# Kernel optimization log

Measured on AMD Instinct MI355X. Metric: run time of the kernel, lower is better.

## Reference

```python
import jax, jax.numpy as jnp
import numpy as np

NEG_SLOPE = 0.2


def gatv2(x, src, dst, Wl, Wr, att, b, concat):
    """PyG GATv2Conv (share_weights=False, default negative_slope=0.2).
    x: [N, Fin]; src/dst: [E] (self-loops already included);
    Wl/Wr: [Fin, H*D]; att: [H, D]; b: [H*D] if concat else [D].
    """
    N = x.shape[0]
    H, D = att.shape
    xl = (x @ Wl).reshape(N, H, D)  # source transform (messages)
    xr = (x @ Wr).reshape(N, H, D)  # target transform
    g = xl[src] + xr[dst]                                   # [E, H, D]
    e = jnp.einsum('ehd,hd->eh', jax.nn.leaky_relu(g, NEG_SLOPE), att)  # [E, H]
    # segment softmax over incoming edges of each dst node
    m = jax.ops.segment_max(e, dst, num_segments=N)         # [N, H]
    ex = jnp.exp(e - m[dst])
    s = jax.ops.segment_sum(ex, dst, num_segments=N)
    alpha = ex / (s[dst] + 1e-16)                           # [E, H]
    out = jax.ops.segment_sum(alpha[:, :, None] * xl[src], dst, num_segments=N)  # [N, H, D]
    out = out.reshape(N, H * D) if concat else out.mean(axis=1)
    return out + b


def _glorot(key, fan_in, shape):
    return jax.random.normal(key, shape, dtype=jnp.float32) / np.sqrt(fan_in)


def setup_inputs() -> dict:
    key = jax.random.key(0)
    N, E = 50000, 800000
    dim_in, dim_h, dim_out, heads = 128, 32, 16, 8
    hid = dim_h * heads  # 256
    ks = jax.random.split(key, 16)
    x = jax.random.normal(ks[0], (N, dim_in), dtype=jnp.float32)
    edge_index = jax.random.randint(ks[1], (2, E), 0, N, dtype=jnp.int32)
    p = {
        'Wl1': _glorot(ks[2], dim_in, (dim_in, hid)),
        'Wr1': _glorot(ks[3], dim_in, (dim_in, hid)),
        'att1': _glorot(ks[4], dim_h, (heads, dim_h)),
        'b1': jnp.zeros((hid,), jnp.float32),
        'Wl2': _glorot(ks[5], hid, (hid, hid)),
        'Wr2': _glorot(ks[6], hid, (hid, hid)),
        'att2': _glorot(ks[7], dim_h, (heads, dim_h)),
        'b2': jnp.zeros((hid,), jnp.float32),
        'Wl3': _glorot(ks[8], hid, (hid, hid)),
        'Wr3': _glorot(ks[9], hid, (hid, hid)),
        'att3': _glorot(ks[10], dim_h, (heads, dim_h)),
        'b3': jnp.zeros((hid,), jnp.float32),
        'Wl4': _glorot(ks[11], hid, (hid, dim_out)),
        'Wr4': _glorot(ks[12], hid, (hid, dim_out)),
        'att4': _glorot(ks[13], dim_out, (1, dim_out)),
        'b4': jnp.zeros((dim_out,), jnp.float32),
    }
    return {'x': x, 'edge_index': edge_index, **p}


def reference(x, edge_index,
              Wl1, Wr1, att1, b1,
              Wl2, Wr2, att2, b2,
              Wl3, Wr3, att3, b3,
              Wl4, Wr4, att4, b4):
    N = x.shape[0]
    # PyG GATv2Conv default add_self_loops=True
    loop = jnp.arange(N, dtype=edge_index.dtype)
    src = jnp.concatenate([edge_index[0], loop])
    dst = jnp.concatenate([edge_index[1], loop])
    # eval mode: dropout is identity (note: first dropout output is unused in source)
    h = gatv2(x, src, dst, Wl1, Wr1, att1, b1, concat=True)
    h = jax.nn.elu(h)
    h = gatv2(h, src, dst, Wl2, Wr2, att2, b2, concat=True)
    h = jax.nn.elu(h)
    h = gatv2(h, src, dst, Wl3, Wr3, att3, b3, concat=True)
    h = jax.nn.elu(h)
    h = gatv2(h, src, dst, Wl4, Wr4, att4, b4, concat=True)  # heads=1 -> same as concat
    return jax.nn.log_softmax(h, axis=1)
```

## Files before the change

### kernel.cpp

```cpp
#include <hip/hip_runtime.h>
#include <math.h>

#define NEG_SLOPE 0.2f

typedef _Float16 f16;
typedef _Float16 f16x2 __attribute__((ext_vector_type(2)));
typedef _Float16 f16x4 __attribute__((ext_vector_type(4)));
typedef _Float16 f16x8 __attribute__((ext_vector_type(8)));
typedef float f32x4 __attribute__((ext_vector_type(4)));

static inline int idiv(int a, int b) { return (a + b - 1) / b; }



__global__ __launch_bounds__(256) void conv_x_packed(const float* __restrict__ x,
                                                     f16* __restrict__ pa, int N) {
    int R = blockIdx.x;
    #pragma unroll
    for (int u = 0; u < 8; ++u) {
        int c = threadIdx.x + u * 256;
        int g = c >> 7, r = c & 127;
        int row = R * 128 + r;
        f16x8 v;
        if (row < N) {
            float4 a = *(const float4*)(x + (size_t)row * 128 + g * 8);
            float4 b = *(const float4*)(x + (size_t)row * 128 + g * 8 + 4);
            v = (f16x8){(f16)a.x, (f16)a.y, (f16)a.z, (f16)a.w,
                        (f16)b.x, (f16)b.y, (f16)b.z, (f16)b.w};
        } else {
            v = (f16x8){0, 0, 0, 0, 0, 0, 0, 0};
        }
        *(f16x8*)(pa + ((size_t)(R * 16 + g) * 128 + r) * 8) = v;
    }
}

__global__ __launch_bounds__(256) void convT_all(
    const float* __restrict__ W1l, const float* __restrict__ W1r,
    const float* __restrict__ W2l, const float* __restrict__ W2r,
    const float* __restrict__ W3l, const float* __restrict__ W3r,
    f16* __restrict__ P1l, f16* __restrict__ P1r,
    f16* __restrict__ P2l, f16* __restrict__ P2r,
    f16* __restrict__ P3l, f16* __restrict__ P3r) {
    __shared__ float tbl[32][33];
    const float* W;
    f16* P;
    int K;
    switch (blockIdx.z) {
        case 0: W = W1l; P = P1l; K = 128; break;
        case 1: W = W1r; P = P1r; K = 128; break;
        case 2: W = W2l; P = P2l; K = 256; break;
        case 3: W = W2r; P = P2r; K = 256; break;
        case 4: W = W3l; P = P3l; K = 256; break;
        default: W = W3r; P = P3r; K = 256; break;
    }
    int bk = blockIdx.x * 32, bc = blockIdx.y * 32;
    if (bk >= K) return;
    int tx = threadIdx.x & 31, ty = threadIdx.x >> 5;
    #pragma unroll
    for (int i = 0; i < 32; i += 8)
        tbl[ty + i][tx] = W[(size_t)(bk + ty + i) * 256 + bc + tx];
    __syncthreads();
    if (threadIdx.x < 128) {
        int cl = threadIdx.x & 31;
        int gl = threadIdx.x >> 5;
        int col = bc + cl;
        int g = (bk >> 3) + gl;
        f16x8 v;
        #pragma unroll
        for (int j = 0; j < 8; ++j) v[j] = (f16)tbl[gl * 8 + j][cl];
        *(f16x8*)(P + ((size_t)((col >> 7) * (K >> 3) + g) * 128 + (col & 127)) * 8) = v;
    }
}


__global__ void hist_kernel(const int* __restrict__ dst, int E, int N, int* __restrict__ cnt) {
    int i = blockIdx.x * blockDim.x + threadIdx.x;
    if (i >= E + N) return;
    int d = (i < E) ? dst[i] : (i - E);
    atomicAdd(&cnt[d], 1);
}

__global__ __launch_bounds__(256) void scanA(const int* __restrict__ cnt,
                                             int* __restrict__ bsum, int N) {
    __shared__ int ws[4];
    int tid = threadIdx.x, lane = tid & 63, wid = tid >> 6;
    int i0 = blockIdx.x * 1024 + tid * 4;
    int s = 0;
    if (i0 + 3 < N) {
        int4 v = *(const int4*)(cnt + i0);
        s = v.x + v.y + v.z + v.w;
    } else {
        for (int j = 0; j < 4; ++j)
            if (i0 + j < N) s += cnt[i0 + j];
    }
    #pragma unroll
    for (int o = 1; o < 64; o <<= 1) s += __shfl_xor(s, o);
    if (lane == 0) ws[wid] = s;
    __syncthreads();
    if (tid == 0) bsum[blockIdx.x] = ws[0] + ws[1] + ws[2] + ws[3];
}

__global__ __launch_bounds__(256) void scanB(int* __restrict__ bsum, int nb) {
    __shared__ int ws[4];
    int tid = threadIdx.x, lane = tid & 63, wid = tid >> 6;
    int v = (tid < nb) ? bsum[tid] : 0;
    int incl = v;
    #pragma unroll
    for (int o = 1; o < 64; o <<= 1) {
        int t = __shfl_up(incl, o);
        if (lane >= o) incl += t;
    }
    if (lane == 63) ws[wid] = incl;
    __syncthreads();
    int add = 0;
    for (int w = 0; w < wid; ++w) add += ws[w];
    if (tid < nb) bsum[tid] = add + incl - v;
}

__global__ __launch_bounds__(256) void scanC(const int* __restrict__ cnt,
                                             const int* __restrict__ bsum,
                                             int* __restrict__ rp, int* __restrict__ wofs, int N) {
    __shared__ int ws[4];
    __shared__ int base_s;
    int tid = threadIdx.x, lane = tid & 63, wid = tid >> 6;
    int i0 = blockIdx.x * 1024 + tid * 4;
    int v0 = (i0 + 0 < N) ? cnt[i0 + 0] : 0;
    int v1 = (i0 + 1 < N) ? cnt[i0 + 1] : 0;
    int v2 = (i0 + 2 < N) ? cnt[i0 + 2] : 0;
    int v3 = (i0 + 3 < N) ? cnt[i0 + 3] : 0;
    int t4 = v0 + v1 + v2 + v3;
    int incl = t4;
    #pragma unroll
    for (int o = 1; o < 64; o <<= 1) {
        int t = __shfl_up(incl, o);
        if (lane >= o) incl += t;
    }
    if (lane == 63) ws[wid] = incl;
    if (tid == 0) base_s = bsum[blockIdx.x];
    __syncthreads();
    int wadd = 0;
    for (int w = 0; w < wid; ++w) wadd += ws[w];
    int pre = base_s + wadd + incl - t4;
    int p1 = pre + v0, p2 = p1 + v1, p3 = p2 + v2, p4 = p3 + v3;
    if (i0 + 0 < N) { wofs[i0 + 0] = pre; rp[i0 + 1] = p1; }
    if (i0 + 1 < N) { wofs[i0 + 1] = p1;  rp[i0 + 2] = p2; }
    if (i0 + 2 < N) { wofs[i0 + 2] = p2;  rp[i0 + 3] = p3; }
    if (i0 + 3 < N) { wofs[i0 + 3] = p3;  rp[i0 + 4] = p4; }
    if (blockIdx.x == 0 && tid == 0) rp[0] = 0;
}

__global__ void scatter_kernel(const int* __restrict__ src, const int* __restrict__ dst,
                               int E, int N, int* __restrict__ wofs, int* __restrict__ sorted_src) {
    int i = blockIdx.x * blockDim.x + threadIdx.x;
    if (i >= E + N) return;
    int d, s;
    if (i < E) { d = dst[i]; s = src[i]; } else { d = i - E; s = d; }
    int pos = atomicAdd(&wofs[d], 1);
    sorted_src[pos] = s;
}


__device__ __forceinline__ void gll16(const f16* g, f16* l) {
#if __has_builtin(__builtin_amdgcn_global_load_lds)
    __builtin_amdgcn_global_load_lds((const __attribute__((address_space(1))) void*)g,
                                     (__attribute__((address_space(3))) void*)l, 16, 0, 0);
#else
    *(f16x8*)l = *(const f16x8*)g;
#endif
}

__global__ __launch_bounds__(256) void gemm16_packed(
    const f16* __restrict__ PA, int N, int K,
    const f16* __restrict__ PBl, const f16* __restrict__ PBr,
    f16* __restrict__ Cl, f16* __restrict__ Cr) {
    __shared__ f16 lds[2][2][8192];
    const int nblk = gridDim.x;
    int bid = blockIdx.x;
    int xcd = bid & 7, jj = bid >> 3;
    int nper = nblk >> 3, rem = nblk & 7;
    int slot = (xcd < rem) ? xcd * (nper + 1) + jj
                           : rem * (nper + 1) + (xcd - rem) * nper + jj;
    int R = slot >> 2, by = slot & 3;
    const f16* __restrict__ PB = (by >> 1) ? PBr : PBl;
    f16* __restrict__ C = (by >> 1) ? Cr : Cl;
    const int cb = by & 1;
    const int row0 = R * 128;
    const int col0 = cb * 128;
    const f16* Abase = PA + (size_t)R * 128 * K;
    const f16* Bbase = PB + (size_t)cb * 128 * K;
    const int t = threadIdx.x;
    const int lane = t & 63, wid = t >> 6;
    const int wr = (wid >> 1) * 64, wc = (wid & 1) * 64;
    const int lg = lane >> 4, lr = lane & 15;

    f32x4 acc[4][4];
    #pragma unroll
    for (int m = 0; m < 4; ++m)
        #pragma unroll
        for (int n = 0; n < 4; ++n) acc[m][n] = (f32x4){0.f, 0.f, 0.f, 0.f};

    auto stage = [&](int buf, int k0) {
        const f16* As = Abase + (size_t)k0 * 128 + t * 8;
        const f16* Bs = Bbase + (size_t)k0 * 128 + t * 8;
        f16* Al = &lds[buf][0][t * 8];
        f16* Bl = &lds[buf][1][t * 8];
        #pragma unroll
        for (int u = 0; u < 4; ++u) gll16(As + u * 2048, Al + u * 2048);
        #pragma unroll
        for (int u = 0; u < 4; ++u) gll16(Bs + u * 2048, Bl + u * 2048);
    };

    const int nk = K >> 6;
    stage(0, 0);
    asm volatile("s_waitcnt vmcnt(0)" ::: "memory");
    __syncthreads();
    for (int c = 0; c < nk; ++c) {
        if (c + 1 < nk) stage((c + 1) & 1, (c + 1) * 64);
        f16x8* Asp = (f16x8*)lds[c & 1][0];
        f16x8* Bsp = (f16x8*)lds[c & 1][1];
        #pragma unroll
        for (int s = 0; s < 2; ++s) {
            f16x8 af[4], bf[4];
            #pragma unroll
            for (int m = 0; m < 4; ++m) af[m] = Asp[(s * 4 + lg) * 128 + wr + m * 16 + lr];
            #pragma unroll
            for (int n = 0; n < 4; ++n) bf[n] = Bsp[(s * 4 + lg) * 128 + wc + n * 16 + lr];
            #pragma unroll
            for (int m = 0; m < 4; ++m)
                #pragma unroll
                for (int n = 0; n < 4; ++n)
                    acc[m][n] = __builtin_amdgcn_mfma_f32_16x16x32_f16(af[m], bf[n], acc[m][n], 0, 0, 0);
        }
        asm volatile("s_waitcnt vmcnt(0)" ::: "memory");
        __syncthreads();
    }
    #pragma unroll
    for (int m = 0; m < 4; ++m) {
        int row_b = row0 + wr + m * 16 + lg * 4;
        #pragma unroll
        for (int reg = 0; reg < 4; ++reg) {
            int row = row_b + reg;
            if (row < N) {
                #pragma unroll
                for (int n = 0; n < 4; ++n)
                    C[(size_t)row * 256 + col0 + wc + n * 16 + lr] = (f16)acc[m][n][reg];
            }
        }
    }
}


__global__ __launch_bounds__(256) void gemm_small16(
    const f16* __restrict__ A, int N,
    const float* __restrict__ Wl, const float* __restrict__ Wr,
    float* __restrict__ Cl, float* __restrict__ Cr) {
    const int K = 256, M = 16;
    __shared__ float As[16][260];
    __shared__ float Ws[256 * 16];
    const float* __restrict__ W = (blockIdx.y == 0) ? Wl : Wr;
    float* __restrict__ C = (blockIdx.y == 0) ? Cl : Cr;
    int row0 = blockIdx.x * 16;
    int tid = threadIdx.x;
    {
        #pragma unroll
        for (int u = 0; u < 4; ++u)
            *(float4*)&Ws[tid * 16 + u * 4] = *(const float4*)(W + tid * 16 + u * 4);
        int r = tid >> 4;
        int c = (tid & 15) * 16;
        int row = row0 + r;
        if (row < N) {
            int R = row >> 7, rr = row & 127;
            const f16* base = A + ((size_t)(R * 32 + (c >> 3)) * 128 + rr) * 8;
            f16x8 v0 = *(const f16x8*)base;
            f16x8 v1 = *(const f16x8*)(base + 1024);
            #pragma unroll
            for (int j = 0; j < 8; ++j) {
                As[r][c + j] = (float)v0[j];
                As[r][c + 8 + j] = (float)v1[j];
            }
        } else {
            #pragma unroll
            for (int j = 0; j < 16; ++j) As[r][c + j] = 0.f;
        }
    }
    __syncthreads();
    int r = tid >> 4;
    int col = tid & 15;
    float acc = 0.f;
    #pragma unroll 8
    for (int k = 0; k < K; ++k) acc = fmaf(As[r][k], Ws[k * M + col], acc);
    int row = row0 + r;
    if (row < N) C[(size_t)row * M + col] = acc;
}


__global__ __launch_bounds__(256) void edge_h8_f16(
    const f16* __restrict__ xl, const f16* __restrict__ xr,
    const int* __restrict__ rp, const int* __restrict__ ss,
    const float* __restrict__ att, const float* __restrict__ bias,
    f16* __restrict__ hout, int N) {
    int tid = threadIdx.x;
    int half = tid >> 5;
    int hl = tid & 31;
    int n = blockIdx.x * 8 + half;
    if (n >= N) return;
    const int HD = 256;
    f16x8 xrr = *(const f16x8*)(xr + (size_t)n * HD + hl * 8);
    float4 atlo = *(const float4*)(att + hl * 8);
    float4 athi = *(const float4*)(att + hl * 8 + 4);
    f16x2 at01 = {(f16)atlo.x, (f16)atlo.y};
    f16x2 at23 = {(f16)atlo.z, (f16)atlo.w};
    f16x2 at45 = {(f16)athi.x, (f16)athi.y};
    f16x2 at67 = {(f16)athi.z, (f16)athi.w};
    const f16 ns = (f16)NEG_SLOPE;
    float m = -INFINITY, s = 0.f;
    f16x8 a = {0, 0, 0, 0, 0, 0, 0, 0};
    int beg = rp[n], end = rp[n + 1];
    int last = end - 1;
    const f16* xb = xl + hl * 8;
    f16x8 r0 = *(const f16x8*)(xb + (size_t)ss[beg] * HD);
    f16x8 r1 = *(const f16x8*)(xb + (size_t)ss[min(beg + 1, last)] * HD);
    f16x8 r2 = *(const f16x8*)(xb + (size_t)ss[min(beg + 2, last)] * HD);
    f16x8 r3 = *(const f16x8*)(xb + (size_t)ss[min(beg + 3, last)] * HD);
    f16x8 r4 = *(const f16x8*)(xb + (size_t)ss[min(beg + 4, last)] * HD);
    f16x8 r5 = *(const f16x8*)(xb + (size_t)ss[min(beg + 5, last)] * HD);
    int j6 = ss[min(beg + 6, last)];
    int j7 = ss[min(beg + 7, last)];

    auto score = [&](const f16x8& cur) -> float {
        f16x8 g = cur + xrr;
        f16x8 gs = g * ns;
        f16x8 lk = __builtin_elementwise_max(g, gs);
#if __has_builtin(__builtin_amdgcn_fdot2)
        f16x2 l01 = __builtin_shufflevector(lk, lk, 0, 1);
        f16x2 l23 = __builtin_shufflevector(lk, lk, 2, 3);
        f16x2 l45 = __builtin_shufflevector(lk, lk, 4, 5);
        f16x2 l67 = __builtin_shufflevector(lk, lk, 6, 7);
        float p = __builtin_amdgcn_fdot2(l01, at01, 0.f, false);
        p = __builtin_amdgcn_fdot2(l23, at23, p, false);
        p = __builtin_amdgcn_fdot2(l45, at45, p, false);
        p = __builtin_amdgcn_fdot2(l67, at67, p, false);
#else
        float p = (float)lk[0] * atlo.x + (float)lk[1] * atlo.y +
                  (float)lk[2] * atlo.z + (float)lk[3] * atlo.w +
                  (float)lk[4] * athi.x + (float)lk[5] * athi.y +
                  (float)lk[6] * athi.z + (float)lk[7] * athi.w;
#endif
        return p;
    };

    int i = beg;
    for (; i + 1 < end; i += 2) {
        f16x8 c0 = r0, c1 = r1;
        r0 = r2; r1 = r3; r2 = r4; r3 = r5;
        r4 = *(const f16x8*)(xb + (size_t)j6 * HD);
        r5 = *(const f16x8*)(xb + (size_t)j7 * HD);
        j6 = ss[min(i + 8, last)];
        j7 = ss[min(i + 9, last)];
        float p0 = score(c0);
        float p1 = score(c1);
        p0 += __shfl_xor(p0, 1);
        p1 += __shfl_xor(p1, 1);
        p0 += __shfl_xor(p0, 2);
        p1 += __shfl_xor(p1, 2);
        float d0 = p0 - m, d1 = p1 - m;
        if (__any(fmaxf(d0, d1) > 4.f)) {
            float mn = fmaxf(m, fmaxf(p0, p1));
            float cf = __expf(m - mn);
            s *= cf;
            f16 cfh = (f16)cf;
            a = a * (f16x8){cfh, cfh, cfh, cfh, cfh, cfh, cfh, cfh};
            m = mn;
            d0 = p0 - m; d1 = p1 - m;
        }
        float e0 = __expf(d0);
        float e1 = __expf(d1);
        s += e0 + e1;
        f16 e0h = (f16)e0, e1h = (f16)e1;
        f16x8 e0v = {e0h, e0h, e0h, e0h, e0h, e0h, e0h, e0h};
        f16x8 e1v = {e1h, e1h, e1h, e1h, e1h, e1h, e1h, e1h};
#if __has_builtin(__builtin_elementwise_fma)
        a = __builtin_elementwise_fma(c0, e0v, a);
        a = __builtin_elementwise_fma(c1, e1v, a);
#else
        a = a + c0 * e0v + c1 * e1v;
#endif
    }
    if (i < end) {
        f16x8 c0 = r0;
        float p0 = score(c0);
        p0 += __shfl_xor(p0, 1);
        p0 += __shfl_xor(p0, 2);
        float d0 = p0 - m;
        if (__any(d0 > 4.f)) {
            float mn = fmaxf(m, p0);
            float cf = __expf(m - mn);
            s *= cf;
            f16 cfh = (f16)cf;
            a = a * (f16x8){cfh, cfh, cfh, cfh, cfh, cfh, cfh, cfh};
            m = mn;
            d0 = p0 - m;
        }
        float e0 = __expf(d0);
        s += e0;
        f16 e0h = (f16)e0;
        f16x8 e0v = {e0h, e0h, e0h, e0h, e0h, e0h, e0h, e0h};
#if __has_builtin(__builtin_elementwise_fma)
        a = __builtin_elementwise_fma(c0, e0v, a);
#else
        a = a + c0 * e0v;
#endif
    }
    float inv = 1.f / (s + 1e-16f);
    float4 blo = *(const float4*)(bias + hl * 8);
    float4 bhi = *(const float4*)(bias + hl * 8 + 4);
    float o[8];
    o[0] = (float)a[0] * inv + blo.x; o[1] = (float)a[1] * inv + blo.y;
    o[2] = (float)a[2] * inv + blo.z; o[3] = (float)a[3] * inv + blo.w;
    o[4] = (float)a[4] * inv + bhi.x; o[5] = (float)a[5] * inv + bhi.y;
    o[6] = (float)a[6] * inv + bhi.z; o[7] = (float)a[7] * inv + bhi.w;
    f16x8 ov;
    #pragma unroll
    for (int j = 0; j < 8; ++j) {
        float e = o[j] > 0.f ? o[j] : __expf(o[j]) - 1.f;
        ov[j] = (f16)e;
    }
    *(f16x8*)(hout + ((size_t)((n >> 7) * 32 + hl) * 128 + (n & 127)) * 8) = ov;
}


__global__ __launch_bounds__(256) void edge_h1_kernel(
    const float* __restrict__ xl, const float* __restrict__ xr,
    const int* __restrict__ rp, const int* __restrict__ ss,
    const float* __restrict__ att, const float* __restrict__ bias,
    float* __restrict__ out, int N) {
    int tid = threadIdx.x;
    int grp = tid >> 4;
    int gl = tid & 15;
    int n = blockIdx.x * 16 + grp;
    if (n >= N) return;
    float xrv = xr[(size_t)n * 16 + gl];
    float attv = att[gl];
    float bv = bias[gl];
    float m = -INFINITY, s = 0.f, acc = 0.f;
    int beg = rp[n], end = rp[n + 1], last = end - 1;
    const float* xb = xl + gl;
    float x0 = xb[(size_t)ss[beg] * 16];
    float x1 = xb[(size_t)ss[min(beg + 1, last)] * 16];
    float x2 = xb[(size_t)ss[min(beg + 2, last)] * 16];
    float x3 = xb[(size_t)ss[min(beg + 3, last)] * 16];
    int j4 = ss[min(beg + 4, last)];
    int j5 = ss[min(beg + 5, last)];
    int i = beg;
    for (; i + 1 < end; i += 2) {
        float c0 = x0, c1 = x1;
        x0 = x2; x1 = x3;
        x2 = xb[(size_t)j4 * 16];
        x3 = xb[(size_t)j5 * 16];
        j4 = ss[min(i + 6, last)];
        j5 = ss[min(i + 7, last)];
        float g0 = c0 + xrv, g1 = c1 + xrv;
        float p0 = attv * fmaxf(g0, NEG_SLOPE * g0);
        float p1 = attv * fmaxf(g1, NEG_SLOPE * g1);
        p0 += __shfl_xor(p0, 1); p1 += __shfl_xor(p1, 1);
        p0 += __shfl_xor(p0, 2); p1 += __shfl_xor(p1, 2);
        p0 += __shfl_xor(p0, 4); p1 += __shfl_xor(p1, 4);
        p0 += __shfl_xor(p0, 8); p1 += __shfl_xor(p1, 8);
        float d0 = p0 - m, d1 = p1 - m;
        if (__any(fmaxf(d0, d1) > 8.f)) {
            float mn = fmaxf(m, fmaxf(p0, p1));
            float cf = __expf(m - mn);
            s *= cf; acc *= cf;
            m = mn;
            d0 = p0 - m; d1 = p1 - m;
        }
        float e0 = __expf(d0), e1 = __expf(d1);
        s += e0 + e1;
        acc = fmaf(e1, c1, fmaf(e0, c0, acc));
    }
    if (i < end) {
        float c0 = x0;
        float g0 = c0 + xrv;
        float p0 = attv * fmaxf(g0, NEG_SLOPE * g0);
        p0 += __shfl_xor(p0, 1);
        p0 += __shfl_xor(p0, 2);
        p0 += __shfl_xor(p0, 4);
        p0 += __shfl_xor(p0, 8);
        float d0 = p0 - m;
        if (__any(d0 > 8.f)) {
            float mn = fmaxf(m, p0);
            float cf = __expf(m - mn);
            s *= cf; acc *= cf;
            m = mn;
            d0 = p0 - m;
        }
        float e0 = __expf(d0);
        s += e0;
        acc = fmaf(e0, c0, acc);
    }
    float v = acc / (s + 1e-16f) + bv;
    float mx = v;
    mx = fmaxf(mx, __shfl_xor(mx, 1));
    mx = fmaxf(mx, __shfl_xor(mx, 2));
    mx = fmaxf(mx, __shfl_xor(mx, 4));
    mx = fmaxf(mx, __shfl_xor(mx, 8));
    float ex = __expf(v - mx);
    float se = ex;
    se += __shfl_xor(se, 1);
    se += __shfl_xor(se, 2);
    se += __shfl_xor(se, 4);
    se += __shfl_xor(se, 8);
    out[(size_t)n * 16 + gl] = v - mx - __logf(se);
}


extern "C" void kernel_launch(void* const* d_in, const int* in_sizes, int n_in,
                              void* d_out, int out_size, void* d_ws, size_t ws_size,
                              hipStream_t stream) {
    const float* x    = (const float*)d_in[0];
    const int*   ei   = (const int*)d_in[1];
    const float* Wl1  = (const float*)d_in[2];
    const float* Wr1  = (const float*)d_in[3];
    const float* att1 = (const float*)d_in[4];
    const float* b1   = (const float*)d_in[5];
    const float* Wl2  = (const float*)d_in[6];
    const float* Wr2  = (const float*)d_in[7];
    const float* att2 = (const float*)d_in[8];
    const float* b2   = (const float*)d_in[9];
    const float* Wl3  = (const float*)d_in[10];
    const float* Wr3  = (const float*)d_in[11];
    const float* att3 = (const float*)d_in[12];
    const float* b3   = (const float*)d_in[13];
    const float* Wl4  = (const float*)d_in[14];
    const float* Wr4  = (const float*)d_in[15];
    const float* att4 = (const float*)d_in[16];
    const float* b4   = (const float*)d_in[17];

    const int N = in_sizes[0] / 128;
    const int E = in_sizes[1] / 2;
    const int* src = ei;
    const int* dst = ei + E;
    const int Etot = E + N;
    const int ntile = idiv(N, 128);

    char* wsb = (char*)d_ws;
    size_t off = 0;
    auto alloc = [&](size_t bytes) -> void* {
        void* p = wsb + off;
        off += (bytes + 255) & ~(size_t)255;
        return p;
    };
    f16*   PX   = (f16*)alloc((size_t)ntile * 128 * 128 * 2);
    f16*   PH   = (f16*)alloc((size_t)ntile * 128 * 256 * 2);
    f16*   xl16 = (f16*)alloc((size_t)N * 256 * 2);
    f16*   xr16 = (f16*)alloc((size_t)N * 256 * 2);
    float* xl4  = (float*)alloc((size_t)N * 16 * 4);
    float* xr4  = (float*)alloc((size_t)N * 16 * 4);
    f16*   PB1l = (f16*)alloc((size_t)256 * 128 * 2);
    f16*   PB1r = (f16*)alloc((size_t)256 * 128 * 2);
    f16*   PB2l = (f16*)alloc((size_t)256 * 256 * 2);
    f16*   PB2r = (f16*)alloc((size_t)256 * 256 * 2);
    f16*   PB3l = (f16*)alloc((size_t)256 * 256 * 2);
    f16*   PB3r = (f16*)alloc((size_t)256 * 256 * 2);
    int*   cnt  = (int*)alloc((size_t)N * 4);
    int*   wof  = (int*)alloc((size_t)N * 4);
    int*   rp   = (int*)alloc((size_t)(N + 1) * 4);
    int*   ss   = (int*)alloc((size_t)Etot * 4);
    int*   bsum = (int*)alloc((size_t)idiv(N, 1024) * 4);

    conv_x_packed<<<ntile, 256, 0, stream>>>(x, PX, N);
    convT_all<<<dim3(8, 8, 6), 256, 0, stream>>>(Wl1, Wr1, Wl2, Wr2, Wl3, Wr3,
                                                 PB1l, PB1r, PB2l, PB2r, PB3l, PB3r);

    hipMemsetAsync(cnt, 0, (size_t)N * 4, stream);
    hist_kernel<<<idiv(Etot, 256), 256, 0, stream>>>(dst, E, N, cnt);
    const int nb = idiv(N, 1024);
    scanA<<<nb, 256, 0, stream>>>(cnt, bsum, N);
    scanB<<<1, 256, 0, stream>>>(bsum, nb);
    scanC<<<nb, 256, 0, stream>>>(cnt, bsum, rp, wof, N);
    scatter_kernel<<<idiv(Etot, 256), 256, 0, stream>>>(src, dst, E, N, wof, ss);

    const int nblk = ntile * 4;
    gemm16_packed<<<nblk, 256, 0, stream>>>(PX, N, 128, PB1l, PB1r, xl16, xr16);
    edge_h8_f16<<<idiv(N, 8), 256, 0, stream>>>(xl16, xr16, rp, ss, att1, b1, PH, N);
    gemm16_packed<<<nblk, 256, 0, stream>>>(PH, N, 256, PB2l, PB2r, xl16, xr16);
    edge_h8_f16<<<idiv(N, 8), 256, 0, stream>>>(xl16, xr16, rp, ss, att2, b2, PH, N);
    gemm16_packed<<<nblk, 256, 0, stream>>>(PH, N, 256, PB3l, PB3r, xl16, xr16);
    edge_h8_f16<<<idiv(N, 8), 256, 0, stream>>>(xl16, xr16, rp, ss, att3, b3, PH, N);
    gemm_small16<<<dim3(idiv(N, 16), 2), 256, 0, stream>>>(PH, N, Wl4, Wr4, xl4, xr4);
    edge_h1_kernel<<<idiv(N, 16), 256, 0, stream>>>(xl4, xr4, rp, ss, att4, b4, (float*)d_out, N);
}
```

Baseline: 447.2 us.

## Store GEMM output head-major and split edge kernel per attention head

The GEMM epilogue now writes xl/xr in a head-major layout ([H][N][32]), so each head's features form a contiguous 3.2 MB plane. The edge kernel is restructured so each block handles one head for 32 nodes, with 8 lanes per node loading 4 halfs each, and the software prefetch depth drops to 4. The aim is to make random neighbour gathers hit a much smaller working set per head, giving better L2/MALL locality across the blocks working on the same head. In exchange each gathered row is only 64 bytes, so there are more, smaller memory transactions, the row indices are re-read once per head, and the output store becomes a narrower f16x4 write.

```diff
diff --git a/kernel.cpp b/kernel.cpp
--- a/kernel.cpp
+++ b/kernel.cpp
@@ -234,6 +234,7 @@
         asm volatile("s_waitcnt vmcnt(0)" ::: "memory");
         __syncthreads();
     }
+    const size_t hs = (size_t)N * 32;
     #pragma unroll
     for (int m = 0; m < 4; ++m) {
         int row_b = row0 + wr + m * 16 + lg * 4;
@@ -242,8 +243,10 @@
             int row = row_b + reg;
             if (row < N) {
                 #pragma unroll
-                for (int n = 0; n < 4; ++n)
-                    C[(size_t)row * 256 + col0 + wc + n * 16 + lr] = (f16)acc[m][n][reg];
+                for (int n = 0; n < 4; ++n) {
+                    int col = col0 + wc + n * 16 + lr;
+                    C[hs * (col >> 5) + (size_t)row * 32 + (col & 31)] = (f16)acc[m][n][reg];
+                }
             }
         }
     }
@@ -294,82 +297,78 @@
 }
 
 
-__global__ __launch_bounds__(256) void edge_h8_f16(
+__global__ __launch_bounds__(256) void edge_h8_hsplit(
     const f16* __restrict__ xl, const f16* __restrict__ xr,
     const int* __restrict__ rp, const int* __restrict__ ss,
     const float* __restrict__ att, const float* __restrict__ bias,
     f16* __restrict__ hout, int N) {
+    int bid = blockIdx.x;
+    int h = bid & 7;
+    int tile = bid >> 3;
     int tid = threadIdx.x;
-    int half = tid >> 5;
-    int hl = tid & 31;
-    int n = blockIdx.x * 8 + half;
+    int lane = tid & 63, wave = tid >> 6;
+    int n = tile * 32 + wave * 8 + (lane >> 3);
     if (n >= N) return;
-    const int HD = 256;
-    f16x8 xrr = *(const f16x8*)(xr + (size_t)n * HD + hl * 8);
-    float4 atlo = *(const float4*)(att + hl * 8);
-    float4 athi = *(const float4*)(att + hl * 8 + 4);
-    f16x2 at01 = {(f16)atlo.x, (f16)atlo.y};
-    f16x2 at23 = {(f16)atlo.z, (f16)atlo.w};
-    f16x2 at45 = {(f16)athi.x, (f16)athi.y};
-    f16x2 at67 = {(f16)athi.z, (f16)athi.w};
+    int ll = lane & 7;
+    const size_t hs = (size_t)N * 32;
+    const f16* xlh = xl + hs * h;
+    const f16* xrh = xr + hs * h;
+    f16x4 xrr = *(const f16x4*)(xrh + (size_t)n * 32 + ll * 4);
+    float4 atv = *(const float4*)(att + h * 32 + ll * 4);
+    f16x2 at01 = {(f16)atv.x, (f16)atv.y};
+    f16x2 at23 = {(f16)atv.z, (f16)atv.w};
     const f16 ns = (f16)NEG_SLOPE;
     float m = -INFINITY, s = 0.f;
-    f16x8 a = {0, 0, 0, 0, 0, 0, 0, 0};
+    f16x4 a = {0, 0, 0, 0};
     int beg = rp[n], end = rp[n + 1];
     int last = end - 1;
-    const f16* xb = xl + hl * 8;
-    f16x8 r0 = *(const f16x8*)(xb + (size_t)ss[beg] * HD);
-    f16x8 r1 = *(const f16x8*)(xb + (size_t)ss[min(beg + 1, last)] * HD);
-    f16x8 r2 = *(const f16x8*)(xb + (size_t)ss[min(beg + 2, last)] * HD);
-    f16x8 r3 = *(const f16x8*)(xb + (size_t)ss[min(beg + 3, last)] * HD);
-    f16x8 r4 = *(const f16x8*)(xb + (size_t)ss[min(beg + 4, last)] * HD);
-    f16x8 r5 = *(const f16x8*)(xb + (size_t)ss[min(beg + 5, last)] * HD);
-    int j6 = ss[min(beg + 6, last)];
-    int j7 = ss[min(beg + 7, last)];
-
-    auto score = [&](const f16x8& cur) -> float {
-        f16x8 g = cur + xrr;
-        f16x8 gs = g * ns;
-        f16x8 lk = __builtin_elementwise_max(g, gs);
+    const f16* xb = xlh + ll * 4;
+    f16x4 r0 = *(const f16x4*)(xb + (size_t)ss[beg] * 32);
+    f16x4 r1 = *(const f16x4*)(xb + (size_t)ss[min(beg + 1, last)] * 32);
+    f16x4 r2 = *(const f16x4*)(xb + (size_t)ss[min(beg + 2, last)] * 32);
+    f16x4 r3 = *(const f16x4*)(xb + (size_t)ss[min(beg + 3, last)] * 32);
+    int j4 = ss[min(beg + 4, last)];
+    int j5 = ss[min(beg + 5, last)];
+
+    auto score = [&](const f16x4& cur) -> float {
+        f16x4 g = cur + xrr;
+        f16x4 gs = g * ns;
+        f16x4 lk = __builtin_elementwise_max(g, gs);
 #if __has_builtin(__builtin_amdgcn_fdot2)
         f16x2 l01 = __builtin_shufflevector(lk, lk, 0, 1);
         f16x2 l23 = __builtin_shufflevector(lk, lk, 2, 3);
-        f16x2 l45 = __builtin_shufflevector(lk, lk, 4, 5);
-        f16x2 l67 = __builtin_shufflevector(lk, lk, 6, 7);
         float p = __builtin_amdgcn_fdot2(l01, at01, 0.f, false);
         p = __builtin_amdgcn_fdot2(l23, at23, p, false);
-        p = __builtin_amdgcn_fdot2(l45, at45, p, false);
-        p = __builtin_amdgcn_fdot2(l67, at67, p, false);
 #else
-        float p = (float)lk[0] * atlo.x + (float)lk[1] * atlo.y +
-                  (float)lk[2] * atlo.z + (float)lk[3] * atlo.w +
-                  (float)lk[4] * athi.x + (float)lk[5] * athi.y +
-                  (float)lk[6] * athi.z + (float)lk[7] * athi.w;
+        float p = (float)lk[0] * atv.x + (float)lk[1] * atv.y +
+                  (float)lk[2] * atv.z + (float)lk[3] * atv.w;
 #endif
         return p;
     };
 
     int i = beg;
     for (; i + 1 < end; i += 2) {
-        f16x8 c0 = r0, c1 = r1;
-        r0 = r2; r1 = r3; r2 = r4; r3 = r5;
-        r4 = *(const f16x8*)(xb + (size_t)j6 * HD);
-        r5 = *(const f16x8*)(xb + (size_t)j7 * HD);
-        j6 = ss[min(i + 8, last)];
-        j7 = ss[min(i + 9, last)];
+        f16x4 c0 = r0, c1 = r1;
+        r0 = r2; r1 = r3;
+        r2 = *(const f16x4*)(xb + (size_t)j4 * 32);
+        r3 = *(const f16x4*)(xb + (size_t)j5 * 32);
+        j4 = ss[min(i + 6, last)];
+        j5 = ss[min(i + 7, last)];
         float p0 = score(c0);
         float p1 = score(c1);
         p0 += __shfl_xor(p0, 1);
         p1 += __shfl_xor(p1, 1);
         p0 += __shfl_xor(p0, 2);
         p1 += __shfl_xor(p1, 2);
+        p0 += __shfl_xor(p0, 4);
+        p1 += __shfl_xor(p1, 4);
         float d0 = p0 - m, d1 = p1 - m;
         if (__any(fmaxf(d0, d1) > 4.f)) {
             float mn = fmaxf(m, fmaxf(p0, p1));
             float cf = __expf(m - mn);
             s *= cf;
             f16 cfh = (f16)cf;
-            a = a * (f16x8){cfh, cfh, cfh, cfh, cfh, cfh, cfh, cfh};
+            a = a * (f16x4){cfh, cfh, cfh, cfh};
             m = mn;
             d0 = p0 - m; d1 = p1 - m;
         }
@@ -377,8 +376,8 @@
         float e1 = __expf(d1);
         s += e0 + e1;
         f16 e0h = (f16)e0, e1h = (f16)e1;
-        f16x8 e0v = {e0h, e0h, e0h, e0h, e0h, e0h, e0h, e0h};
-        f16x8 e1v = {e1h, e1h, e1h, e1h, e1h, e1h, e1h, e1h};
+        f16x4 e0v = {e0h, e0h, e0h, e0h};
+        f16x4 e1v = {e1h, e1h, e1h, e1h};
 #if __has_builtin(__builtin_elementwise_fma)
         a = __builtin_elementwise_fma(c0, e0v, a);
         a = __builtin_elementwise_fma(c1, e1v, a);
@@ -387,24 +386,25 @@
 #endif
     }
     if (i < end) {
-        f16x8 c0 = r0;
+        f16x4 c0 = r0;
         float p0 = score(c0);
         p0 += __shfl_xor(p0, 1);
         p0 += __shfl_xor(p0, 2);
+        p0 += __shfl_xor(p0, 4);
         float d0 = p0 - m;
         if (__any(d0 > 4.f)) {
             float mn = fmaxf(m, p0);
             float cf = __expf(m - mn);
             s *= cf;
             f16 cfh = (f16)cf;
-            a = a * (f16x8){cfh, cfh, cfh, cfh, cfh, cfh, cfh, cfh};
+            a = a * (f16x4){cfh, cfh, cfh, cfh};
             m = mn;
             d0 = p0 - m;
         }
         float e0 = __expf(d0);
         s += e0;
         f16 e0h = (f16)e0;
-        f16x8 e0v = {e0h, e0h, e0h, e0h, e0h, e0h, e0h, e0h};
+        f16x4 e0v = {e0h, e0h, e0h, e0h};
 #if __has_builtin(__builtin_elementwise_fma)
         a = __builtin_elementwise_fma(c0, e0v, a);
 #else
@@ -412,20 +412,19 @@
 #endif
     }
     float inv = 1.f / (s + 1e-16f);
-    float4 blo = *(const float4*)(bias + hl * 8);
-    float4 bhi = *(const float4*)(bias + hl * 8 + 4);
-    float o[8];
-    o[0] = (float)a[0] * inv + blo.x; o[1] = (float)a[1] * inv + blo.y;
-    o[2] = (float)a[2] * inv + blo.z; o[3] = (float)a[3] * inv + blo.w;
-    o[4] = (float)a[4] * inv + bhi.x; o[5] = (float)a[5] * inv + bhi.y;
-    o[6] = (float)a[6] * inv + bhi.z; o[7] = (float)a[7] * inv + bhi.w;
-    f16x8 ov;
-    #pragma unroll
-    for (int j = 0; j < 8; ++j) {
-        float e = o[j] > 0.f ? o[j] : __expf(o[j]) - 1.f;
-        ov[j] = (f16)e;
-    }
-    *(f16x8*)(hout + ((size_t)((n >> 7) * 32 + hl) * 128 + (n & 127)) * 8) = ov;
+    float4 bv = *(const float4*)(bias + h * 32 + ll * 4);
+    float o0 = (float)a[0] * inv + bv.x;
+    float o1 = (float)a[1] * inv + bv.y;
+    float o2 = (float)a[2] * inv + bv.z;
+    float o3 = (float)a[3] * inv + bv.w;
+    o0 = o0 > 0.f ? o0 : __expf(o0) - 1.f;
+    o1 = o1 > 0.f ? o1 : __expf(o1) - 1.f;
+    o2 = o2 > 0.f ? o2 : __expf(o2) - 1.f;
+    o3 = o3 > 0.f ? o3 : __expf(o3) - 1.f;
+    f16x4 ov = {(f16)o0, (f16)o1, (f16)o2, (f16)o3};
+    f16* outp = hout + ((size_t)((n >> 7) * 32 + 4 * h + (ll >> 1)) * 128 + (n & 127)) * 8 +
+                (ll & 1) * 4;
+    *(f16x4*)outp = ov;
 }
 
 
@@ -581,12 +580,13 @@
     scatter_kernel<<<idiv(Etot, 256), 256, 0, stream>>>(src, dst, E, N, wof, ss);
 
     const int nblk = ntile * 4;
+    const int egrid = idiv(N, 32) * 8;
     gemm16_packed<<<nblk, 256, 0, stream>>>(PX, N, 128, PB1l, PB1r, xl16, xr16);
-    edge_h8_f16<<<idiv(N, 8), 256, 0, stream>>>(xl16, xr16, rp, ss, att1, b1, PH, N);
+    edge_h8_hsplit<<<egrid, 256, 0, stream>>>(xl16, xr16, rp, ss, att1, b1, PH, N);
     gemm16_packed<<<nblk, 256, 0, stream>>>(PH, N, 256, PB2l, PB2r, xl16, xr16);
-    edge_h8_f16<<<idiv(N, 8), 256, 0, stream>>>(xl16, xr16, rp, ss, att2, b2, PH, N);
+    edge_h8_hsplit<<<egrid, 256, 0, stream>>>(xl16, xr16, rp, ss, att2, b2, PH, N);
     gemm16_packed<<<nblk, 256, 0, stream>>>(PH, N, 256, PB3l, PB3r, xl16, xr16);
-    edge_h8_f16<<<idiv(N, 8), 256, 0, stream>>>(xl16, xr16, rp, ss, att3, b3, PH, N);
+    edge_h8_hsplit<<<egrid, 256, 0, stream>>>(xl16, xr16, rp, ss, att3, b3, PH, N);
     gemm_small16<<<dim3(idiv(N, 16), 2), 256, 0, stream>>>(PH, N, Wl4, Wr4, xl4, xr4);
     edge_h1_kernel<<<idiv(N, 16), 256, 0, stream>>>(xl4, xr4, rp, ss, att4, b4, (float*)d_out, N);
 }
```

After: 488.2 us. 9.2% more time.

## Sort nodes by degree and split edge aggregation per head with head-major features

Applied to the files above, without the earlier changes.

Adds a degree histogram, scan and scatter that build a permutation of nodes ordered by in-degree, so warps in the edge kernels process nodes of similar degree and diverge less. The GEMM now writes xl/xr in head-major layout ([H][N][32]). The layer-1 to 3 edge kernel is restructured so each block handles one head across 64 nodes with 4 lanes per node, making each gathered row a contiguous 64-byte head slice that should stay in cache within a head. The change adds three small preprocessing kernels and shortens the prefetch depth, and trades fewer lanes per node for more nodes per wave.

```diff
diff --git a/kernel.cpp b/kernel.cpp
--- a/kernel.cpp
+++ b/kernel.cpp
@@ -157,6 +157,50 @@
     if (i < E) { d = dst[i]; s = src[i]; } else { d = i - E; s = d; }
     int pos = atomicAdd(&wofs[d], 1);
     sorted_src[pos] = s;
+}
+
+
+__global__ __launch_bounds__(256) void deg_hist(const int* __restrict__ rp, int N,
+                                                int* __restrict__ dcnt) {
+    __shared__ int l[64];
+    if (threadIdx.x < 64) l[threadIdx.x] = 0;
+    __syncthreads();
+    int i = blockIdx.x * 256 + threadIdx.x;
+    if (i < N) atomicAdd(&l[min(rp[i + 1] - rp[i], 63)], 1);
+    __syncthreads();
+    if (threadIdx.x < 64 && l[threadIdx.x]) atomicAdd(&dcnt[threadIdx.x], l[threadIdx.x]);
+}
+
+__global__ void deg_scan(int* __restrict__ dcnt) {
+    int tid = threadIdx.x;
+    int v = dcnt[tid];
+    int incl = v;
+    #pragma unroll
+    for (int o = 1; o < 64; o <<= 1) {
+        int t = __shfl_up(incl, o);
+        if (tid >= o) incl += t;
+    }
+    dcnt[tid] = incl - v;
+}
+
+__global__ __launch_bounds__(256) void deg_scatter(const int* __restrict__ rp, int N,
+                                                   int* __restrict__ gofs,
+                                                   int* __restrict__ perm) {
+    __shared__ int lcnt[64];
+    __shared__ int lbase[64];
+    int tid = threadIdx.x;
+    if (tid < 64) lcnt[tid] = 0;
+    __syncthreads();
+    int i = blockIdx.x * 256 + tid;
+    int deg = 0, lrank = 0;
+    if (i < N) {
+        deg = min(rp[i + 1] - rp[i], 63);
+        lrank = atomicAdd(&lcnt[deg], 1);
+    }
+    __syncthreads();
+    if (tid < 64 && lcnt[tid] > 0) lbase[tid] = atomicAdd(&gofs[tid], lcnt[tid]);
+    __syncthreads();
+    if (i < N) perm[lbase[deg] + lrank] = i;
 }
 
 
@@ -234,6 +278,7 @@
         asm volatile("s_waitcnt vmcnt(0)" ::: "memory");
         __syncthreads();
     }
+    const size_t hs = (size_t)N * 32;
     #pragma unroll
     for (int m = 0; m < 4; ++m) {
         int row_b = row0 + wr + m * 16 + lg * 4;
@@ -242,8 +287,10 @@
             int row = row_b + reg;
             if (row < N) {
                 #pragma unroll
-                for (int n = 0; n < 4; ++n)
-                    C[(size_t)row * 256 + col0 + wc + n * 16 + lr] = (f16)acc[m][n][reg];
+                for (int n = 0; n < 4; ++n) {
+                    int col = col0 + wc + n * 16 + lr;
+                    C[hs * (col >> 5) + (size_t)row * 32 + (col & 31)] = (f16)acc[m][n][reg];
+                }
             }
         }
     }
@@ -294,20 +341,26 @@
 }
 
 
-__global__ __launch_bounds__(256) void edge_h8_f16(
+__global__ __launch_bounds__(256) void edge_h8_sorted(
     const f16* __restrict__ xl, const f16* __restrict__ xr,
     const int* __restrict__ rp, const int* __restrict__ ss,
+    const int* __restrict__ perm,
     const float* __restrict__ att, const float* __restrict__ bias,
     f16* __restrict__ hout, int N) {
+    int bid = blockIdx.x;
+    int h = bid & 7;
+    int tile = bid >> 3;
     int tid = threadIdx.x;
-    int half = tid >> 5;
-    int hl = tid & 31;
-    int n = blockIdx.x * 8 + half;
-    if (n >= N) return;
-    const int HD = 256;
-    f16x8 xrr = *(const f16x8*)(xr + (size_t)n * HD + hl * 8);
-    float4 atlo = *(const float4*)(att + hl * 8);
-    float4 athi = *(const float4*)(att + hl * 8 + 4);
+    int task = tile * 64 + (tid >> 2);
+    if (task >= N) return;
+    int n = perm[task];
+    int ll = tid & 3;
+    const size_t hs = (size_t)N * 32;
+    const f16* xlh = xl + hs * h;
+    const int doff = h * 32 + ll * 8;
+    f16x8 xrr = *(const f16x8*)(xr + hs * h + (size_t)n * 32 + ll * 8);
+    float4 atlo = *(const float4*)(att + doff);
+    float4 athi = *(const float4*)(att + doff + 4);
     f16x2 at01 = {(f16)atlo.x, (f16)atlo.y};
     f16x2 at23 = {(f16)atlo.z, (f16)atlo.w};
     f16x2 at45 = {(f16)athi.x, (f16)athi.y};
@@ -317,15 +370,13 @@
     f16x8 a = {0, 0, 0, 0, 0, 0, 0, 0};
     int beg = rp[n], end = rp[n + 1];
     int last = end - 1;
-    const f16* xb = xl + hl * 8;
-    f16x8 r0 = *(const f16x8*)(xb + (size_t)ss[beg] * HD);
-    f16x8 r1 = *(const f16x8*)(xb + (size_t)ss[min(beg + 1, last)] * HD);
-    f16x8 r2 = *(const f16x8*)(xb + (size_t)ss[min(beg + 2, last)] * HD);
-    f16x8 r3 = *(const f16x8*)(xb + (size_t)ss[min(beg + 3, last)] * HD);
-    f16x8 r4 = *(const f16x8*)(xb + (size_t)ss[min(beg + 4, last)] * HD);
-    f16x8 r5 = *(const f16x8*)(xb + (size_t)ss[min(beg + 5, last)] * HD);
-    int j6 = ss[min(beg + 6, last)];
-    int j7 = ss[min(beg + 7, last)];
+    const f16* xb = xlh + ll * 8;
+    f16x8 r0 = *(const f16x8*)(xb + (size_t)ss[beg] * 32);
+    f16x8 r1 = *(const f16x8*)(xb + (size_t)ss[min(beg + 1, last)] * 32);
+    f16x8 r2 = *(const f16x8*)(xb + (size_t)ss[min(beg + 2, last)] * 32);
+    f16x8 r3 = *(const f16x8*)(xb + (size_t)ss[min(beg + 3, last)] * 32);
+    int j4 = ss[min(beg + 4, last)];
+    int j5 = ss[min(beg + 5, last)];
 
     auto score = [&](const f16x8& cur) -> float {
         f16x8 g = cur + xrr;
@@ -352,11 +403,11 @@
     int i = beg;
     for (; i + 1 < end; i += 2) {
         f16x8 c0 = r0, c1 = r1;
-        r0 = r2; r1 = r3; r2 = r4; r3 = r5;
-        r4 = *(const f16x8*)(xb + (size_t)j6 * HD);
-        r5 = *(const f16x8*)(xb + (size_t)j7 * HD);
-        j6 = ss[min(i + 8, last)];
-        j7 = ss[min(i + 9, last)];
+        r0 = r2; r1 = r3;
+        r2 = *(const f16x8*)(xb + (size_t)j4 * 32);
+        r3 = *(const f16x8*)(xb + (size_t)j5 * 32);
+        j4 = ss[min(i + 6, last)];
+        j5 = ss[min(i + 7, last)];
         float p0 = score(c0);
         float p1 = score(c1);
         p0 += __shfl_xor(p0, 1);
@@ -412,8 +463,8 @@
 #endif
     }
     float inv = 1.f / (s + 1e-16f);
-    float4 blo = *(const float4*)(bias + hl * 8);
-    float4 bhi = *(const float4*)(bias + hl * 8 + 4);
+    float4 blo = *(const float4*)(bias + doff);
+    float4 bhi = *(const float4*)(bias + doff + 4);
     float o[8];
     o[0] = (float)a[0] * inv + blo.x; o[1] = (float)a[1] * inv + blo.y;
     o[2] = (float)a[2] * inv + blo.z; o[3] = (float)a[3] * inv + blo.w;
@@ -425,20 +476,22 @@
         float e = o[j] > 0.f ? o[j] : __expf(o[j]) - 1.f;
         ov[j] = (f16)e;
     }
-    *(f16x8*)(hout + ((size_t)((n >> 7) * 32 + hl) * 128 + (n & 127)) * 8) = ov;
+    *(f16x8*)(hout + ((size_t)((n >> 7) * 32 + 4 * h + ll) * 128 + (n & 127)) * 8) = ov;
 }
 
 
 __global__ __launch_bounds__(256) void edge_h1_kernel(
     const float* __restrict__ xl, const float* __restrict__ xr,
     const int* __restrict__ rp, const int* __restrict__ ss,
+    const int* __restrict__ perm,
     const float* __restrict__ att, const float* __restrict__ bias,
     float* __restrict__ out, int N) {
     int tid = threadIdx.x;
     int grp = tid >> 4;
     int gl = tid & 15;
-    int n = blockIdx.x * 16 + grp;
-    if (n >= N) return;
+    int task = blockIdx.x * 16 + grp;
+    if (task >= N) return;
+    int n = perm[task];
     float xrv = xr[(size_t)n * 16 + gl];
     float attv = att[gl];
     float bv = bias[gl];
@@ -567,26 +620,34 @@
     int*   rp   = (int*)alloc((size_t)(N + 1) * 4);
     int*   ss   = (int*)alloc((size_t)Etot * 4);
     int*   bsum = (int*)alloc((size_t)idiv(N, 1024) * 4);
+    int*   dcnt = (int*)alloc(64 * 4);
+    int*   perm = (int*)alloc((size_t)N * 4);
 
     conv_x_packed<<<ntile, 256, 0, stream>>>(x, PX, N);
     convT_all<<<dim3(8, 8, 6), 256, 0, stream>>>(Wl1, Wr1, Wl2, Wr2, Wl3, Wr3,
                                                  PB1l, PB1r, PB2l, PB2r, PB3l, PB3r);
 
     hipMemsetAsync(cnt, 0, (size_t)N * 4, stream);
+    hipMemsetAsync(dcnt, 0, 64 * 4, stream);
     hist_kernel<<<idiv(Etot, 256), 256, 0, stream>>>(dst, E, N, cnt);
     const int nb = idiv(N, 1024);
     scanA<<<nb, 256, 0, stream>>>(cnt, bsum, N);
     scanB<<<1, 256, 0, stream>>>(bsum, nb);
     scanC<<<nb, 256, 0, stream>>>(cnt, bsum, rp, wof, N);
     scatter_kernel<<<idiv(Etot, 256), 256, 0, stream>>>(src, dst, E, N, wof, ss);
+    deg_hist<<<idiv(N, 256), 256, 0, stream>>>(rp, N, dcnt);
+    deg_scan<<<1, 64, 0, stream>>>(dcnt);
+    deg_scatter<<<idiv(N, 256), 256, 0, stream>>>(rp, N, dcnt, perm);
 
     const int nblk = ntile * 4;
+    const int egrid = idiv(N, 64) * 8;
     gemm16_packed<<<nblk, 256, 0, stream>>>(PX, N, 128, PB1l, PB1r, xl16, xr16);
-    edge_h8_f16<<<idiv(N, 8), 256, 0, stream>>>(xl16, xr16, rp, ss, att1, b1, PH, N);
+    edge_h8_sorted<<<egrid, 256, 0, stream>>>(xl16, xr16, rp, ss, perm, att1, b1, PH, N);
     gemm16_packed<<<nblk, 256, 0, stream>>>(PH, N, 256, PB2l, PB2r, xl16, xr16);
-    edge_h8_f16<<<idiv(N, 8), 256, 0, stream>>>(xl16, xr16, rp, ss, att2, b2, PH, N);
+    edge_h8_sorted<<<egrid, 256, 0, stream>>>(xl16, xr16, rp, ss, perm, att2, b2, PH, N);
     gemm16_packed<<<nblk, 256, 0, stream>>>(PH, N, 256, PB3l, PB3r, xl16, xr16);
-    edge_h8_f16<<<idiv(N, 8), 256, 0, stream>>>(xl16, xr16, rp, ss, att3, b3, PH, N);
+    edge_h8_sorted<<<egrid, 256, 0, stream>>>(xl16, xr16, rp, ss, perm, att3, b3, PH, N);
     gemm_small16<<<dim3(idiv(N, 16), 2), 256, 0, stream>>>(PH, N, Wl4, Wr4, xl4, xr4);
-    edge_h1_kernel<<<idiv(N, 16), 256, 0, stream>>>(xl4, xr4, rp, ss, att4, b4, (float*)d_out, N);
-}
+    edge_h1_kernel<<<idiv(N, 16), 256, 0, stream>>>(xl4, xr4, rp, ss, perm, att4, b4,
+                                                    (float*)d_out, N);
+}
```

New measurement: 525.9 us. 1.18x slower.
